# Kernel optimization log

Measured on AMD Instinct MI355X. Metric: run time of the kernel, lower is better.

The kernel has to match this reference:

```python
import jax, jax.numpy as jnp
import numpy as np

N_NODES = 20000
N_EDGES = 160000
F_IN = 256
N_CLASSES = 32
HEADS = 8
GAT_C = 128


def setup_inputs() -> dict:
    key = jax.random.key(0)
    ks = jax.random.split(key, 20)

    def w(k, shape, fan_in):
        return jax.random.normal(k, shape, dtype=jnp.float32) * (1.0 / np.sqrt(fan_in))

    return {
        "x": jax.random.normal(ks[0], (N_NODES, F_IN), dtype=jnp.float32),
        "edge_index": jax.random.randint(ks[1], (2, N_EDGES), 0, N_NODES, dtype=jnp.int64),
        # SAGEConv(256 -> 64): lin_l (bias) on aggregated neighbors, lin_r (no bias) on root
        "W_l1": w(ks[2], (F_IN, 64), F_IN), "b_l1": jnp.zeros((64,), jnp.float32),
        "W_r1": w(ks[3], (F_IN, 64), F_IN),
        # SAGEConv(64 -> 128)
        "W_l2": w(ks[4], (64, 128), 64), "b_l2": jnp.zeros((128,), jnp.float32),
        "W_r2": w(ks[5], (64, 128), 64),
        # GATConv(128 -> 128, heads=8, concat)
        "W_g": w(ks[6], (128, HEADS * GAT_C), 128),
        "att_src": w(ks[7], (HEADS, GAT_C), GAT_C),
        "att_dst": w(ks[8], (HEADS, GAT_C), GAT_C),
        "b_g": jnp.zeros((HEADS * GAT_C,), jnp.float32),
        # GCNConv(1024 -> 64), GCNConv(64 -> 32)
        "W_c1": w(ks[9], (HEADS * GAT_C, 64), HEADS * GAT_C), "b_c1": jnp.zeros((64,), jnp.float32),
        "W_c2": w(ks[10], (64, N_CLASSES), 64), "b_c2": jnp.zeros((N_CLASSES,), jnp.float32),
        # residual Linear(256 -> 64)
        "W_res": w(ks[11], (F_IN, 64), F_IN), "b_res": jnp.zeros((64,), jnp.float32),
    }


def _forward(x, edge_index, W_l1, b_l1, W_r1, W_l2, b_l2, W_r2,
             W_g, att_src, att_dst, b_g, W_c1, b_c1, W_c2, b_c2, W_res, b_res):
    n = x.shape[0]
    src, dst = edge_index[0], edge_index[1]  # messages flow src -> dst

    def sage(h, Wl, bl, Wr):
        # mean aggregation of neighbor features, then lin_l(agg) + lin_r(root)
        s = jax.ops.segment_sum(h[src], dst, num_segments=n)
        cnt = jax.ops.segment_sum(jnp.ones_like(src, dtype=h.dtype), dst, num_segments=n)
        mean = s / jnp.maximum(cnt, 1.0)[:, None]
        return mean @ Wl + bl + h @ Wr

    res_x = x @ W_res + b_res
    h = jax.nn.relu(sage(x, W_l1, b_l1, W_r1)) + res_x      # [N, 64]
    h = jax.nn.relu(sage(h, W_l2, b_l2, W_r2))              # [N, 128]

    # ---- GATConv with self-loops (PyG default) ----
    loop = jnp.arange(n, dtype=src.dtype)
    srcf = jnp.concatenate([src, loop])
    dstf = jnp.concatenate([dst, loop])

    hg = (h @ W_g).reshape(n, HEADS, GAT_C)                 # [N, H, C]
    a_s = jnp.sum(hg * att_src, axis=-1)                    # [N, H]
    a_d = jnp.sum(hg * att_dst, axis=-1)                    # [N, H]
    e = jax.nn.leaky_relu(a_s[srcf] + a_d[dstf], negative_slope=0.2)  # [Ef, H]
    m = jax.ops.segment_max(e, dstf, num_segments=n)
    e = jnp.exp(e - m[dstf])
    denom = jax.ops.segment_sum(e, dstf, num_segments=n)
    alpha = e / denom[dstf]                                 # softmax over incoming edges
    gat = jax.ops.segment_sum(alpha[:, :, None] * hg[srcf], dstf, num_segments=n)
    h = jax.nn.relu(gat.reshape(n, HEADS * GAT_C) + b_g)    # [N, 1024]

    # ---- GCNConv with self-loops and symmetric normalization ----
    deg = jax.ops.segment_sum(jnp.ones_like(srcf, dtype=h.dtype), dstf, num_segments=n)
    dinv = jax.lax.rsqrt(jnp.maximum(deg, 1.0))             # deg >= 1 via self-loops
    norm = (dinv[srcf] * dinv[dstf])[:, None]

    def gcn(h, W, b):
        hw = h @ W
        return jax.ops.segment_sum(norm * hw[srcf], dstf, num_segments=n) + b

    h = gcn(h, W_c1, b_c1)
    h = gcn(h, W_c2, b_c2)
    return jax.nn.log_softmax(h, axis=1)


def reference(x, edge_index, W_l1, b_l1, W_r1, W_l2, b_l2, W_r2,
              W_g, att_src, att_dst, b_g, W_c1, b_c1, W_c2, b_c2, W_res, b_res):
    return _forward(x, edge_index, W_l1, b_l1, W_r1, W_l2, b_l2, W_r2,
                    W_g, att_src, att_dst, b_g, W_c1, b_c1, W_c2, b_c2, W_res, b_res)
```

## Files before the change

kernel.cpp:

```cpp
#include <hip/hip_runtime.h>

#define NN 20000
#define NE 160000
#define NEF 180000
#define NB1 ((NN + 255) / 256)

typedef long long ll;
typedef __attribute__((ext_vector_type(4))) float f32x4;
typedef __attribute__((ext_vector_type(8))) short s16x8;

static __device__ __forceinline__ float b2f(ushort u) {
  return __uint_as_float(((unsigned)u) << 16);
}
static __device__ __forceinline__ ushort f2b(float f) {
  unsigned u = __float_as_uint(f);
  return (ushort)((u + 0x7fffu + ((u >> 16) & 1u)) >> 16);
}

template<int MF, int NF, int K, bool F32OUT>
__global__ __launch_bounds__(256) void gemm_mfma(
    const ushort* __restrict__ A, const ushort* __restrict__ Bt,
    const float* __restrict__ bias, void* __restrict__ Cv,
    int M, int N, int lda)
{
  const int wid  = threadIdx.x >> 6;
  const int lane = threadIdx.x & 63;
  const int wr = wid >> 1, wc = wid & 1;
  const int bm = blockIdx.y * (32 * MF) + wr * (16 * MF);
  const int bn = blockIdx.x * (32 * NF) + wc * (16 * NF);
  const int lr = lane & 15;
  const int ko = (lane >> 4) * 8;

  const ushort* pa[MF];
  const ushort* pb[NF];
  #pragma unroll
  for (int i = 0; i < MF; i++) {
    int r = min(bm + i * 16 + lr, M - 1);
    pa[i] = A + (ll)r * lda + ko;
  }
  #pragma unroll
  for (int j = 0; j < NF; j++) {
    int c = min(bn + j * 16 + lr, N - 1);
    pb[j] = Bt + (ll)c * K + ko;
  }

  f32x4 acc[MF][NF];
  #pragma unroll
  for (int i = 0; i < MF; i++)
    #pragma unroll
    for (int j = 0; j < NF; j++) acc[i][j] = {0.f, 0.f, 0.f, 0.f};

  #pragma unroll
  for (int k = 0; k < K; k += 32) {
    s16x8 af[MF], bf[NF];
    #pragma unroll
    for (int i = 0; i < MF; i++) af[i] = *(const s16x8*)(pa[i] + k);
    #pragma unroll
    for (int j = 0; j < NF; j++) bf[j] = *(const s16x8*)(pb[j] + k);
    #pragma unroll
    for (int i = 0; i < MF; i++)
      #pragma unroll
      for (int j = 0; j < NF; j++)
        acc[i][j] = __builtin_amdgcn_mfma_f32_16x16x32_bf16(af[i], bf[j], acc[i][j], 0, 0, 0);
  }

  const int rq = (lane >> 4) * 4;
  #pragma unroll
  for (int i = 0; i < MF; i++) {
    #pragma unroll
    for (int j = 0; j < NF; j++) {
      int col = bn + j * 16 + lr;
      if (col >= N) continue;
      float bv = bias ? bias[col] : 0.f;
      int rbase = bm + i * 16 + rq;
      #pragma unroll
      for (int r = 0; r < 4; r++) {
        int row = rbase + r;
        if (row >= M) continue;
        float v = acc[i][j][r] + bv;
        if (F32OUT) ((float*)Cv)[(ll)row * N + col] = v;
        else        ((ushort*)Cv)[(ll)row * N + col] = f2b(v);
      }
    }
  }
}

__global__ __launch_bounds__(256) void k_gat_apply_gcn1(
    const ushort* __restrict__ agg,
    const ushort* __restrict__ BtG,
    const ushort* __restrict__ Btc1,
    const float* __restrict__ b_g,
    ushort* __restrict__ hw64)
{
  __shared__ ushort At[2][32 * 128];
  __shared__ ushort gt[2][32][72];
  const int t    = threadIdx.x;
  const int wc   = t >> 6;
  const int lane = t & 63;
  const int bm = blockIdx.x * 32;
  const int lr = lane & 15;
  const int q  = lane >> 4;
  const int ko = q * 8;
  const int rq = q * 4;

  const int srow = t >> 3;
  const int scg  = t & 7;
  const ushort* sg = agg + (ll)min(bm + srow, NN - 1) * 1024 + scg * 16;
  const int w0 = srow * 128 + (((2 * scg)     ^ (srow & 7)) * 8);
  const int w1 = srow * 128 + (((2 * scg + 1) ^ (srow & 7)) * 8);

  s16x8 ar[8][2];
  #pragma unroll
  for (int h = 0; h < 8; h++) {
    ar[h][0] = *(const s16x8*)(sg + h * 128);
    ar[h][1] = *(const s16x8*)(sg + h * 128 + 8);
  }

  s16x8 b1[2][4];
  s16x8 b2[2][2];
  float bvs[2];
  {
    const int cg = wc * 16 + lr;
    const ushort* pb = BtG + (ll)cg * 128 + ko;
    b1[0][0] = *(const s16x8*)(pb);
    b1[0][1] = *(const s16x8*)(pb + 32);
    b1[0][2] = *(const s16x8*)(pb + 64);
    b1[0][3] = *(const s16x8*)(pb + 96);
    const ushort* qb = Btc1 + (ll)cg * 1024 + ko;
    b2[0][0] = *(const s16x8*)(qb);
    b2[0][1] = *(const s16x8*)(qb + 32);
    bvs[0] = b_g[cg];
  }

  f32x4 o0 = {0.f, 0.f, 0.f, 0.f}, o1 = o0;

  #pragma unroll
  for (int h = 0; h < 8; h++) {
    *(s16x8*)&At[h & 1][w0] = ar[h][0];
    *(s16x8*)&At[h & 1][w1] = ar[h][1];
    __syncthreads();
    #pragma unroll
    for (int it = 0; it < 2; it++) {
      const int ct = 2 * h + it;
      const int cur = it, nxt = it ^ 1;
      if (ct < 15) {
        const int cg2 = (ct + 1) * 64 + wc * 16 + lr;
        const ushort* pb2 = BtG + (ll)cg2 * 128 + ko;
        b1[nxt][0] = *(const s16x8*)(pb2);
        b1[nxt][1] = *(const s16x8*)(pb2 + 32);
        b1[nxt][2] = *(const s16x8*)(pb2 + 64);
        b1[nxt][3] = *(const s16x8*)(pb2 + 96);
        const ushort* qb2 = Btc1 + (ll)(wc * 16 + lr) * 1024 + (ct + 1) * 64 + ko;
        b2[nxt][0] = *(const s16x8*)(qb2);
        b2[nxt][1] = *(const s16x8*)(qb2 + 32);
        bvs[nxt] = b_g[cg2];
      }
      f32x4 g0 = {0.f, 0.f, 0.f, 0.f}, g1 = g0;
      #pragma unroll
      for (int k = 0; k < 4; k++) {
        const int gi = (k * 4 + q) ^ (lr & 7);
        s16x8 a0 = *(const s16x8*)&At[h & 1][lr        * 128 + gi * 8];
        s16x8 a1 = *(const s16x8*)&At[h & 1][(16 + lr) * 128 + gi * 8];
        g0 = __builtin_amdgcn_mfma_f32_16x16x32_bf16(a0, b1[cur][k], g0, 0, 0, 0);
        g1 = __builtin_amdgcn_mfma_f32_16x16x32_bf16(a1, b1[cur][k], g1, 0, 0, 0);
      }
      float bv = bvs[cur];
      #pragma unroll
      for (int r = 0; r < 4; r++) {
        gt[it][rq + r][wc * 16 + lr]      = f2b(fmaxf(g0[r] + bv, 0.f));
        gt[it][16 + rq + r][wc * 16 + lr] = f2b(fmaxf(g1[r] + bv, 0.f));
      }
      __syncthreads();
      {
        s16x8 a0 = *(const s16x8*)&gt[it][lr][ko];
        s16x8 a1 = *(const s16x8*)&gt[it][16 + lr][ko];
        o0 = __builtin_amdgcn_mfma_f32_16x16x32_bf16(a0, b2[cur][0], o0, 0, 0, 0);
        o1 = __builtin_amdgcn_mfma_f32_16x16x32_bf16(a1, b2[cur][0], o1, 0, 0, 0);
        s16x8 a2 = *(const s16x8*)&gt[it][lr][32 + ko];
        s16x8 a3 = *(const s16x8*)&gt[it][16 + lr][32 + ko];
        o0 = __builtin_amdgcn_mfma_f32_16x16x32_bf16(a2, b2[cur][1], o0, 0, 0, 0);
        o1 = __builtin_amdgcn_mfma_f32_16x16x32_bf16(a3, b2[cur][1], o1, 0, 0, 0);
      }
    }
  }
  int col = wc * 16 + lr;
  #pragma unroll
  for (int r = 0; r < 4; r++) {
    int row0 = bm + rq + r, row1 = bm + 16 + rq + r;
    if (row0 < NN) hw64[(ll)row0 * 64 + col] = f2b(o0[r]);
    if (row1 < NN) hw64[(ll)row1 * 64 + col] = f2b(o1[r]);
  }
}

struct PrepEnt { const float* W; ushort* Bt; int N; int K; int base; };
struct Prep { PrepEnt e[8]; int total; };

__global__ void k_setup(const float* __restrict__ x, ushort* __restrict__ xb, Prep p,
                        const float* __restrict__ b_res, const float* __restrict__ b_l1,
                        const float* __restrict__ b_l2, float* __restrict__ bias192,
                        float* __restrict__ bias256,
                        const float* __restrict__ W_g, const float* __restrict__ att_s,
                        const float* __restrict__ att_d, ushort* __restrict__ watt_t,
                        int* __restrict__ icnt) {
  ll t = (ll)blockIdx.x * 256 + threadIdx.x;
  const ll T0 = (ll)NN * 64;
  if (t < T0) {
    ll i = t * 4;
    float4 v = *(const float4*)(x + i);
    ushort4 o;
    o.x = f2b(v.x); o.y = f2b(v.y); o.z = f2b(v.z); o.w = f2b(v.w);
    *(ushort4*)(xb + i) = o;
    return;
  }
  t -= T0;
  if (t < p.total) {
    int tt = (int)t;
    #pragma unroll
    for (int i = 0; i < 8; i++) {
      int sz = p.e[i].N * p.e[i].K;
      if (tt >= p.e[i].base && tt < p.e[i].base + sz) {
        int loc = tt - p.e[i].base;
        int n = loc / p.e[i].K, k = loc - n * p.e[i].K;
        p.e[i].Bt[loc] = f2b(p.e[i].W[(ll)k * p.e[i].N + n]);
      }
    }
    return;
  }
  t -= p.total;
  if (t < 256) {
    int tt = (int)t;
    if (tt < 64) bias192[tt] = b_res[tt];
    else if (tt < 128) bias192[tt] = 0.f;
    else if (tt < 192) bias192[tt] = b_l1[tt - 128];
    bias256[tt] = (tt < 128) ? 0.f : b_l2[tt - 128];
    return;
  }
  t -= 256;
  if (t < 2048) {
    int k = (int)t >> 4;
    int col = (int)t & 15;
    int h = col & 7;
    const float* av = (col < 8) ? (att_s + h * 128) : (att_d + h * 128);
    const float* wrow = W_g + (ll)k * 1024 + h * 128;
    float s = 0.f;
    for (int j = 0; j < 128; j++) s += wrow[j] * av[j];
    watt_t[col * 128 + k] = f2b(s);
    return;
  }
  t -= 2048;
  if (t < NN) icnt[t] = 0;
}

__global__ void k_counti(const int* __restrict__ dst, int* __restrict__ icnt) {
  int e = blockIdx.x * 256 + threadIdx.x;
  if (e < NE) atomicAdd(&icnt[dst[e]], 1);
}

__global__ __launch_bounds__(256) void k_scan1(const int* __restrict__ icnt,
                                               int* __restrict__ rowptr,
                                               int* __restrict__ bsum) {
  __shared__ int sd[256];
  int t = threadIdx.x;
  int i = blockIdx.x * 256 + t;
  int v = (i < NN) ? icnt[i] + 1 : 0;
  sd[t] = v;
  __syncthreads();
  #pragma unroll
  for (int o = 1; o < 256; o <<= 1) {
    int u = (t >= o) ? sd[t - o] : 0;
    __syncthreads();
    sd[t] += u;
    __syncthreads();
  }
  if (i < NN) rowptr[i] = sd[t] - v;
  if (t == 255) bsum[blockIdx.x] = sd[255];
}

__global__ __launch_bounds__(128) void k_scan2(const int* __restrict__ bsum,
                                               int* __restrict__ boff) {
  __shared__ int sd[128];
  int t = threadIdx.x;
  int v = (t < NB1) ? bsum[t] : 0;
  sd[t] = v;
  __syncthreads();
  #pragma unroll
  for (int o = 1; o < 128; o <<= 1) {
    int u = (t >= o) ? sd[t - o] : 0;
    __syncthreads();
    sd[t] += u;
    __syncthreads();
  }
  if (t < NB1) boff[t] = sd[t] - v;
}

__global__ void k_scan3(int* __restrict__ rowptr, const int* __restrict__ boff,
                        int* __restrict__ cur, const int* __restrict__ icnt,
                        float* __restrict__ dinv) {
  int i = blockIdx.x * 256 + threadIdx.x;
  if (i >= NN) return;
  int r = rowptr[i] + boff[i >> 8];
  rowptr[i] = r;
  cur[i] = r;
  dinv[i] = rsqrtf((float)icnt[i] + 1.0f);
  if (i == 0) rowptr[NN] = NEF;
}

__global__ void k_scatter(const int* __restrict__ dst, int* __restrict__ cur,
                          int* __restrict__ eid) {
  int t = blockIdx.x * 256 + threadIdx.x;
  if (t >= NEF) return;
  int d = (t < NE) ? dst[t] : t - NE;
  int p = atomicAdd(&cur[d], 1);
  eid[p] = t;
}

template<int C, int STRIDE, bool ADD_RES>
__global__ __launch_bounds__(256) void k_sage_csr(
    const int* __restrict__ rowptr, const int* __restrict__ eid,
    const int* __restrict__ src, const ushort* __restrict__ feat,
    const ushort* __restrict__ linr, const ushort* __restrict__ resx,
    ushort* __restrict__ out)
{
  int node = blockIdx.x * 4 + (threadIdx.x >> 6);
  int lane = threadIdx.x & 63;
  if (node >= NN) return;
  int b = rowptr[node], e = rowptr[node + 1];
  float a0 = 0.f, a1 = 0.f;
  int n = 0;
  for (int base = b; base < e; base += 64) {
    int m = min(64, e - base);
    int sreg = -1;
    if (lane < m) {
      int ed = eid[base + lane];
      sreg = (ed < NE) ? src[ed] : -1;
    }
    for (int i = 0; i < m; i++) {
      int s = __shfl(sreg, i);
      if (s >= 0) {
        a0 += b2f(feat[(ll)s * STRIDE + lane]);
        if (C == 128) a1 += b2f(feat[(ll)s * STRIDE + lane + 64]);
        n++;
      }
    }
  }
  float inv = 1.f / fmaxf((float)n, 1.f);
  {
    float v = a0 * inv + b2f(linr[(ll)node * STRIDE + lane]);
    v = fmaxf(v, 0.f);
    if (ADD_RES) v += b2f(resx[(ll)node * STRIDE + lane]);
    out[(ll)node * C + lane] = f2b(v);
  }
  if (C == 128) {
    float v = a1 * inv + b2f(linr[(ll)node * STRIDE + lane + 64]);
    v = fmaxf(v, 0.f);
    out[(ll)node * C + lane + 64] = f2b(v);
  }
}

__global__ __launch_bounds__(128) void k_gat_agg(
    const int* __restrict__ rowptr, const int* __restrict__ eid,
    const int* __restrict__ src, const float* __restrict__ asd,
    const ushort* __restrict__ h2b, ushort* __restrict__ agg)
{
  __shared__ int s_l[64];
  __shared__ float al[64 * 8];
  __shared__ float adl[8];
  __shared__ float mrun[8], srun[8], fac[8];
  int node = blockIdx.x;
  int c = threadIdx.x;
  int b = rowptr[node], e = rowptr[node + 1];
  if (c < 8) {
    adl[c] = asd[(ll)node * 16 + 8 + c];
    mrun[c] = -3.0e38f;
    srun[c] = 0.f;
  }
  float acc[8] = {0.f, 0.f, 0.f, 0.f, 0.f, 0.f, 0.f, 0.f};
  for (int c0 = b; c0 < e; c0 += 64) {
    int m = min(64, e - c0);
    if (c < m) { int ed = eid[c0 + c]; s_l[c] = (ed < NE) ? src[ed] : node; }
    __syncthreads();
    for (int idx = c; idx < m * 8; idx += 128) {
      int i = idx >> 3, h = idx & 7;
      float v = asd[(ll)s_l[i] * 16 + h] + adl[h];
      al[idx] = (v > 0.f) ? v : 0.2f * v;
    }
    __syncthreads();
    if (c < 8) {
      float cm = mrun[c];
      for (int i = 0; i < m; i++) cm = fmaxf(cm, al[i * 8 + c]);
      fac[c] = __expf(mrun[c] - cm);
      mrun[c] = cm;
    }
    __syncthreads();
    for (int idx = c; idx < m * 8; idx += 128) {
      int h = idx & 7;
      al[idx] = __expf(al[idx] - mrun[h]);
    }
    __syncthreads();
    if (c < 8) {
      float cs = 0.f;
      for (int i = 0; i < m; i++) cs += al[i * 8 + c];
      srun[c] = srun[c] * fac[c] + cs;
    }
    #pragma unroll
    for (int h = 0; h < 8; h++) acc[h] *= fac[h];
    for (int i = 0; i < m; i++) {
      float v = b2f(h2b[(ll)s_l[i] * 128 + c]);
      float4 aa = *(const float4*)&al[i * 8];
      float4 ab = *(const float4*)&al[i * 8 + 4];
      acc[0] = fmaf(aa.x, v, acc[0]);
      acc[1] = fmaf(aa.y, v, acc[1]);
      acc[2] = fmaf(aa.z, v, acc[2]);
      acc[3] = fmaf(aa.w, v, acc[3]);
      acc[4] = fmaf(ab.x, v, acc[4]);
      acc[5] = fmaf(ab.y, v, acc[5]);
      acc[6] = fmaf(ab.z, v, acc[6]);
      acc[7] = fmaf(ab.w, v, acc[7]);
    }
    __syncthreads();
  }
  #pragma unroll
  for (int h = 0; h < 8; h++)
    agg[(ll)node * 1024 + h * 128 + c] = f2b(acc[h] / srun[h]);
}

template<int C, bool FUSE_LSM>
__global__ __launch_bounds__(256) void k_gcn_csr(
    const int* __restrict__ rowptr, const int* __restrict__ eid,
    const int* __restrict__ src, const float* __restrict__ dinv,
    const ushort* __restrict__ hw, const float* __restrict__ bias,
    void* __restrict__ outv)
{
  const int npb = 256 / C;
  int node = blockIdx.x * npb + threadIdx.x / C;
  int c = threadIdx.x & (C - 1);
  if (node >= NN) return;
  int b = rowptr[node], e = rowptr[node + 1];
  float acc = 0.f;
  for (int base = b; base < e; base += C) {
    int m = min(C, e - base);
    int sreg = 0;
    float dreg = 0.f;
    if (c < m) {
      int ed = eid[base + c];
      sreg = (ed < NE) ? src[ed] : node;
      dreg = dinv[sreg];
    }
    for (int i = 0; i < m; i++) {
      int s  = __shfl(sreg, i, C);
      float dv = __shfl(dreg, i, C);
      acc = fmaf(dv, b2f(hw[(ll)s * C + c]), acc);
    }
  }
  float v = acc * dinv[node] + bias[c];
  if (!FUSE_LSM) {
    ((ushort*)outv)[(ll)node * C + c] = f2b(v);
  } else {
    float mx = v;
    #pragma unroll
    for (int o = 16; o > 0; o >>= 1) mx = fmaxf(mx, __shfl_xor(mx, o, 32));
    float s = expf(v - mx);
    #pragma unroll
    for (int o = 16; o > 0; o >>= 1) s += __shfl_xor(s, o, 32);
    ((float*)outv)[(ll)node * C + c] = v - mx - logf(s);
  }
}

extern "C" void kernel_launch(void* const* d_in, const int* in_sizes, int n_in,
                              void* d_out, int out_size, void* d_ws, size_t ws_size,
                              hipStream_t stream) {
  const float* x     = (const float*)d_in[0];
  const int*   ei    = (const int*)d_in[1];
  const float* W_l1  = (const float*)d_in[2];
  const float* b_l1  = (const float*)d_in[3];
  const float* W_r1  = (const float*)d_in[4];
  const float* W_l2  = (const float*)d_in[5];
  const float* b_l2  = (const float*)d_in[6];
  const float* W_r2  = (const float*)d_in[7];
  const float* W_g   = (const float*)d_in[8];
  const float* att_s = (const float*)d_in[9];
  const float* att_d = (const float*)d_in[10];
  const float* b_g   = (const float*)d_in[11];
  const float* W_c1  = (const float*)d_in[12];
  const float* b_c1  = (const float*)d_in[13];
  const float* W_c2  = (const float*)d_in[14];
  const float* b_c2  = (const float*)d_in[15];
  const float* W_res = (const float*)d_in[16];
  const float* b_res = (const float*)d_in[17];
  const int* src = ei;
  const int* dst = ei + NE;
  float* out = (float*)d_out;

  float* Wf = (float*)d_ws;
  size_t off = 0;
  auto take = [&](size_t n) { float* p = Wf + off; off += (n + 3) & ~(size_t)3; return p; };
  ushort* xb    = (ushort*)take((size_t)NN * 128);
  ushort* C192  = (ushort*)take((size_t)NN * 96);
  ushort* h1    = (ushort*)take((size_t)NN * 32);
  ushort* C256  = (ushort*)take((size_t)NN * 128);
  ushort* h2    = (ushort*)take((size_t)NN * 64);
  ushort* agg   = (ushort*)take((size_t)NN * 512);
  ushort* hw64  = (ushort*)take((size_t)NN * 32);
  ushort* acc64 = (ushort*)take((size_t)NN * 32);
  ushort* hw32  = (ushort*)take((size_t)NN * 16);
  ushort* Bt192 = (ushort*)take(192 * 256 / 2);
  ushort* Bt256 = (ushort*)take(256 * 64 / 2);
  ushort* BtG   = (ushort*)take(1024 * 128 / 2);
  ushort* Btc1  = (ushort*)take(64 * 1024 / 2);
  ushort* Btc2  = (ushort*)take(32 * 64 / 2);
  ushort* watt_t= (ushort*)take(16 * 128 / 2);
  float* bias192 = take(192);
  float* bias256 = take(256);
  int*   icnt   = (int*)take(NN);
  int*   rowptr = (int*)take(NN + 1);
  int*   cur    = (int*)take(NN);
  int*   eidb   = (int*)take(NEF);
  int*   bsum   = (int*)take(NB1);
  int*   boff   = (int*)take(NB1);
  float* dinv   = take(NN);
  float* asd    = take((size_t)NN * 16);
  (void)ws_size; (void)in_sizes; (void)n_in; (void)out_size;

  auto nb = [](ll t) { return dim3((unsigned)((t + 255) / 256)); };

  Prep pp;
  int base = 0;
  auto ent = [&](int i, const float* W, ushort* Bt, int N_, int K_) {
    pp.e[i] = {W, Bt, N_, K_, base}; base += N_ * K_;
  };
  ent(0, W_res, Bt192,             64, 256);
  ent(1, W_l1,  Bt192 + 64 * 256,  64, 256);
  ent(2, W_r1,  Bt192 + 128 * 256, 64, 256);
  ent(3, W_l2,  Bt256,             128, 64);
  ent(4, W_r2,  Bt256 + 128 * 64,  128, 64);
  ent(5, W_g,   BtG,               1024, 128);
  ent(6, W_c1,  Btc1,              64, 1024);
  ent(7, W_c2,  Btc2,              32, 64);
  pp.total = base;
  k_setup<<<nb((ll)NN * 64 + base + 256 + 2048 + NN), 256, 0, stream>>>(
      x, xb, pp, b_res, b_l1, b_l2, bias192, bias256, W_g, att_s, att_d, watt_t, icnt);

  k_counti<<<nb(NE), 256, 0, stream>>>(dst, icnt);
  k_scan1<<<NB1, 256, 0, stream>>>(icnt, rowptr, bsum);
  k_scan2<<<1, 128, 0, stream>>>(bsum, boff);
  k_scan3<<<nb(NN), 256, 0, stream>>>(rowptr, boff, cur, icnt, dinv);
  k_scatter<<<nb(NEF), 256, 0, stream>>>(dst, cur, eidb);

  gemm_mfma<4, 2, 256, false><<<dim3(3, 157), 256, 0, stream>>>(
      xb, Bt192, bias192, C192, NN, 192, 256);
  k_sage_csr<64, 192, true><<<nb((ll)NN * 64), 256, 0, stream>>>(
      rowptr, eidb, src, C192 + 64, C192 + 128, C192, h1);

  gemm_mfma<4, 2, 64, false><<<dim3(4, 157), 256, 0, stream>>>(
      h1, Bt256, bias256, C256, NN, 256, 64);
  k_sage_csr<128, 256, false><<<nb((ll)NN * 64), 256, 0, stream>>>(
      rowptr, eidb, src, C256, C256 + 128, nullptr, h2);

  gemm_mfma<4, 1, 128, true><<<dim3(1, 157), 256, 0, stream>>>(
      h2, watt_t, nullptr, asd, NN, 16, 128);
  k_gat_agg<<<dim3(NN), 128, 0, stream>>>(
      rowptr, eidb, src, asd, h2, agg);
  k_gat_apply_gcn1<<<dim3(625), 256, 0, stream>>>(agg, BtG, Btc1, b_g, hw64);
  k_gcn_csr<64, false><<<nb((ll)NN * 64), 256, 0, stream>>>(
      rowptr, eidb, src, dinv, hw64, b_c1, acc64);

  gemm_mfma<4, 1, 64, false><<<dim3(1, 157), 256, 0, stream>>>(
      acc64, Btc2, nullptr, hw32, NN, 32, 64);
  k_gcn_csr<32, true><<<nb((ll)NN * 32), 256, 0, stream>>>(
      rowptr, eidb, src, dinv, hw32, b_c2, out);
}
```

Baseline: 219.2 us.

## Fuse attention-score GEMM into SAGE epilogue and GCN2 weight into GCN1 epilogue

Attention source/destination scores are now computed in the second SAGE aggregation kernel's epilogue, using the attention weights staged in shared memory and a wave reduction. The small GEMM after the first GCN aggregation is folded into that kernel's epilogue through lane shuffles. Together these remove two small GEMM launches and the round trips of h2 and acc64 through memory. In exchange the aggregation kernels carry extra shared-memory loads, a block barrier and 16 serial wave reductions per node. The in-epilogue matmuls also change the rounding path slightly.

```diff
diff --git a/kernel.cpp b/kernel.cpp
--- a/kernel.cpp
+++ b/kernel.cpp
@@ -314,13 +314,19 @@
   eid[p] = t;
 }
 
-template<int C, int STRIDE, bool ADD_RES>
+template<int C, int STRIDE, bool ADD_RES, bool SCORES>
 __global__ __launch_bounds__(256) void k_sage_csr(
     const int* __restrict__ rowptr, const int* __restrict__ eid,
     const int* __restrict__ src, const ushort* __restrict__ feat,
     const ushort* __restrict__ linr, const ushort* __restrict__ resx,
-    ushort* __restrict__ out)
+    ushort* __restrict__ out, const ushort* __restrict__ watt,
+    float* __restrict__ asd)
 {
+  __shared__ ushort wat[2048];
+  if (SCORES) {
+    for (int i = threadIdx.x; i < 2048; i += 256) wat[i] = watt[i];
+    __syncthreads();
+  }
   int node = blockIdx.x * 4 + (threadIdx.x >> 6);
   int lane = threadIdx.x & 63;
   if (node >= NN) return;
@@ -344,16 +350,24 @@
     }
   }
   float inv = 1.f / fmaxf((float)n, 1.f);
-  {
-    float v = a0 * inv + b2f(linr[(ll)node * STRIDE + lane]);
-    v = fmaxf(v, 0.f);
-    if (ADD_RES) v += b2f(resx[(ll)node * STRIDE + lane]);
-    out[(ll)node * C + lane] = f2b(v);
-  }
+  float v0 = a0 * inv + b2f(linr[(ll)node * STRIDE + lane]);
+  v0 = fmaxf(v0, 0.f);
+  if (ADD_RES) v0 += b2f(resx[(ll)node * STRIDE + lane]);
+  out[(ll)node * C + lane] = f2b(v0);
+  float v1 = 0.f;
   if (C == 128) {
-    float v = a1 * inv + b2f(linr[(ll)node * STRIDE + lane + 64]);
-    v = fmaxf(v, 0.f);
-    out[(ll)node * C + lane + 64] = f2b(v);
+    v1 = a1 * inv + b2f(linr[(ll)node * STRIDE + lane + 64]);
+    v1 = fmaxf(v1, 0.f);
+    out[(ll)node * C + lane + 64] = f2b(v1);
+  }
+  if (SCORES && C == 128) {
+    #pragma unroll
+    for (int j = 0; j < 16; j++) {
+      float p = v0 * b2f(wat[j * 128 + lane]) + v1 * b2f(wat[j * 128 + lane + 64]);
+      #pragma unroll
+      for (int o = 32; o > 0; o >>= 1) p += __shfl_down(p, o);
+      if (lane == 0) asd[(ll)node * 16 + j] = p;
+    }
   }
 }
 
@@ -424,13 +438,18 @@
     agg[(ll)node * 1024 + h * 128 + c] = f2b(acc[h] / srun[h]);
 }
 
-template<int C, bool FUSE_LSM>
+template<int C, bool FUSE_LSM, bool FUSE_C2>
 __global__ __launch_bounds__(256) void k_gcn_csr(
     const int* __restrict__ rowptr, const int* __restrict__ eid,
     const int* __restrict__ src, const float* __restrict__ dinv,
     const ushort* __restrict__ hw, const float* __restrict__ bias,
-    void* __restrict__ outv)
+    void* __restrict__ outv, const ushort* __restrict__ w2)
 {
+  __shared__ ushort w2l[2048];
+  if (FUSE_C2) {
+    for (int i = threadIdx.x; i < 2048; i += 256) w2l[i] = w2[i];
+    __syncthreads();
+  }
   const int npb = 256 / C;
   int node = blockIdx.x * npb + threadIdx.x / C;
   int c = threadIdx.x & (C - 1);
@@ -453,7 +472,17 @@
     }
   }
   float v = acc * dinv[node] + bias[c];
-  if (!FUSE_LSM) {
+  if (FUSE_C2) {
+    int j = c & 31, half = c >> 5;
+    float part = 0.f;
+    #pragma unroll 8
+    for (int i = 0; i < 32; i++) {
+      float vv = __shfl(v, half * 32 + i, 64);
+      part = fmaf(vv, b2f(w2l[j * 64 + half * 32 + i]), part);
+    }
+    part += __shfl_xor(part, 32, 64);
+    if (c < 32) ((ushort*)outv)[(ll)node * 32 + j] = f2b(part);
+  } else if (!FUSE_LSM) {
     ((ushort*)outv)[(ll)node * C + c] = f2b(v);
   } else {
     float mx = v;
@@ -501,7 +530,6 @@
   ushort* h2    = (ushort*)take((size_t)NN * 64);
   ushort* agg   = (ushort*)take((size_t)NN * 512);
   ushort* hw64  = (ushort*)take((size_t)NN * 32);
-  ushort* acc64 = (ushort*)take((size_t)NN * 32);
   ushort* hw32  = (ushort*)take((size_t)NN * 16);
   ushort* Bt192 = (ushort*)take(192 * 256 / 2);
   ushort* Bt256 = (ushort*)take(256 * 64 / 2);
@@ -548,24 +576,20 @@
 
   gemm_mfma<4, 2, 256, false><<<dim3(3, 157), 256, 0, stream>>>(
       xb, Bt192, bias192, C192, NN, 192, 256);
-  k_sage_csr<64, 192, true><<<nb((ll)NN * 64), 256, 0, stream>>>(
-      rowptr, eidb, src, C192 + 64, C192 + 128, C192, h1);
+  k_sage_csr<64, 192, true, false><<<nb((ll)NN * 64), 256, 0, stream>>>(
+      rowptr, eidb, src, C192 + 64, C192 + 128, C192, h1, nullptr, nullptr);
 
   gemm_mfma<4, 2, 64, false><<<dim3(4, 157), 256, 0, stream>>>(
       h1, Bt256, bias256, C256, NN, 256, 64);
-  k_sage_csr<128, 256, false><<<nb((ll)NN * 64), 256, 0, stream>>>(
-      rowptr, eidb, src, C256, C256 + 128, nullptr, h2);
-
-  gemm_mfma<4, 1, 128, true><<<dim3(1, 157), 256, 0, stream>>>(
-      h2, watt_t, nullptr, asd, NN, 16, 128);
+  k_sage_csr<128, 256, false, true><<<nb((ll)NN * 64), 256, 0, stream>>>(
+      rowptr, eidb, src, C256, C256 + 128, nullptr, h2, watt_t, asd);
+
   k_gat_agg<<<dim3(NN), 128, 0, stream>>>(
       rowptr, eidb, src, asd, h2, agg);
   k_gat_apply_gcn1<<<dim3(625), 256, 0, stream>>>(agg, BtG, Btc1, b_g, hw64);
-  k_gcn_csr<64, false><<<nb((ll)NN * 64), 256, 0, stream>>>(
-      rowptr, eidb, src, dinv, hw64, b_c1, acc64);
-
-  gemm_mfma<4, 1, 64, false><<<dim3(1, 157), 256, 0, stream>>>(
-      acc64, Btc2, nullptr, hw32, NN, 32, 64);
-  k_gcn_csr<32, true><<<nb((ll)NN * 32), 256, 0, stream>>>(
-      rowptr, eidb, src, dinv, hw32, b_c2, out);
-}
+
+  k_gcn_csr<64, false, true><<<nb((ll)NN * 64), 256, 0, stream>>>(
+      rowptr, eidb, src, dinv, hw64, b_c1, hw32, Btc2);
+  k_gcn_csr<32, true, false><<<nb((ll)NN * 32), 256, 0, stream>>>(
+      rowptr, eidb, src, dinv, hw32, b_c2, out, nullptr);
+}
```

Result: slower. 234.4 us (+6.9%).
